# Optimization experiments

Measured on AMD Instinct MI355X. Metric: run time of the kernel, lower is better.

The kernel has to match this reference:

```python
import jax, jax.numpy as jnp
import numpy as np

EPS = 1e-5

def _hdc_branch(emb, w, b, dil, ln_g, ln_b):
    # emb: [N, L, E]; w: [K, E, F] ('WIO'); same-length dilated conv
    y = jax.lax.conv_general_dilated(
        emb, w, window_strides=(1,), padding=[(dil, dil)],
        rhs_dilation=(dil,), dimension_numbers=('NWC', 'WIO', 'NWC')) + b
    m = y.mean(-1, keepdims=True)
    v = ((y - m) ** 2).mean(-1, keepdims=True)
    y = (y - m) / jnp.sqrt(v + EPS) * ln_g + ln_b
    return jax.nn.relu(y)  # [N, L, F]

def _news_encoder(titles, embedding, w1, b1, w2, b2, w3, b3, ln_g, ln_b,
                  q_levels, q_words):
    B, n, L = titles.shape
    E = embedding.shape[-1]
    emb = embedding[titles].reshape(B * n, L, E)  # dropout = identity (eval)
    d = jnp.stack([
        _hdc_branch(emb, w1, b1, 1, ln_g, ln_b),
        _hdc_branch(emb, w2, b2, 2, ln_g, ln_b),
        _hdc_branch(emb, w3, b3, 3, ln_g, ln_b),
    ], axis=2)  # [Bn, L, 3, F]
    F = d.shape[-1]
    d = d.reshape(B, n, L, 3, F)
    scale = jnp.sqrt(jnp.asarray(E, d.dtype))  # original divides by sqrt(embedding_dim)
    # level-wise attention pooling (1-row query over 3 levels)
    wl = jax.nn.softmax(jnp.einsum('f,bnlkf->bnlk', q_levels[0], d) / scale, axis=-1)
    attn = jnp.einsum('bnlk,bnlkf->bnlf', wl, d)  # [B, n, L, F]
    # word-wise attention pooling (1-row query over L words)
    ww = jax.nn.softmax(jnp.einsum('f,bnlf->bnl', q_words[0], attn) / scale, axis=-1)
    reprs = jnp.einsum('bnl,bnlf->bnf', ww, attn)  # [B, n, F]
    return reprs

def setup_inputs() -> dict:
    key = jax.random.key(0)
    ks = jax.random.split(key, 12)
    V, E, F, H = 50000, 300, 150, 50
    return {
        'candidate_title': jax.random.randint(ks[0], (64, 5, 30), 0, V),
        'clicked_title': jax.random.randint(ks[1], (64, H, 30), 0, V),
        'embedding': jax.random.normal(ks[2], (V, E), jnp.float32),
        'w1': jax.random.normal(ks[3], (3, E, F), jnp.float32) * 0.05,
        'b1': jax.random.normal(ks[4], (F,), jnp.float32) * 0.05,
        'w2': jax.random.normal(ks[5], (3, E, F), jnp.float32) * 0.05,
        'b2': jax.random.normal(ks[6], (F,), jnp.float32) * 0.05,
        'w3': jax.random.normal(ks[7], (3, E, F), jnp.float32) * 0.05,
        'b3': jax.random.normal(ks[8], (F,), jnp.float32) * 0.05,
        'ln_g': jnp.ones((F,), jnp.float32),
        'ln_b': jnp.zeros((F,), jnp.float32),
        'q_levels': jax.random.normal(ks[9], (1, F), jnp.float32),
        'q_words': jax.random.normal(ks[10], (1, F), jnp.float32),
        'ltr_w': jax.random.normal(ks[11], (1, H), jnp.float32) * 0.1,
        'ltr_b': jnp.zeros((1,), jnp.float32),
    }

def reference(candidate_title, clicked_title, embedding, w1, b1, w2, b2, w3, b3,
              ln_g, ln_b, q_levels, q_words, ltr_w, ltr_b):
    cdd = _news_encoder(candidate_title, embedding, w1, b1, w2, b2, w3, b3,
                        ln_g, ln_b, q_levels, q_words)  # [B, cdd, F]
    his = _news_encoder(clicked_title, embedding, w1, b1, w2, b2, w3, b3,
                        ln_g, ln_b, q_levels, q_words)  # [B, his, F]
    scores = jnp.einsum('bcf,bhf->bch', cdd, his)        # [B, cdd, his]
    logits = jnp.einsum('bch,oh->bco', scores, ltr_w)[..., 0] + ltr_b[0]  # [B, cdd]
    return jax.nn.log_softmax(logits, axis=1)  # cdd_size > 1 branch
```

## Files before the change

kernel.cpp:

```cpp
#include <hip/hip_runtime.h>

typedef unsigned short u16;
typedef unsigned int   u32;
typedef __bf16 bf16x8 __attribute__((ext_vector_type(8)));
typedef float  f32x4  __attribute__((ext_vector_type(4)));
typedef _Float16 h2 __attribute__((ext_vector_type(2)));

#define M_ROWS 50000
#define M_PAD  50176
#define M_TILES 196
#define N_REAL 1368
#define N_PAD  1536
#define N_TILES 11
#define K_DIM  300
#define K_PAD  320
#define KT     10
#define TROW   1408
#define SEG    152
#define YCOL   152
#define TS     136

#define GLDS(gp, lp) __builtin_amdgcn_global_load_lds( \
    (const __attribute__((address_space(1))) void*)(gp), \
    (__attribute__((address_space(3))) void*)(lp), 16, 0, 0)

static __device__ __forceinline__ u16 f2bf(float x){
  union { float f; u32 u; } a; a.f = x;
  u32 r = a.u + 0x7fffu + ((a.u >> 16) & 1u);
  return (u16)(r >> 16);
}
static __device__ __forceinline__ u16 f2h(float x){
  _Float16 h = (_Float16)x;
  u16 r; __builtin_memcpy(&r, &h, 2); return r;
}
static __device__ __forceinline__ float h2f(u16 v){
  _Float16 h; __builtin_memcpy(&h, &v, 2); return (float)h;
}

static __device__ __forceinline__ float wsum63(float x){
  asm volatile(
    "s_nop 1\n\t"
    "v_add_f32 %0, %0, %0 row_shr:1 bound_ctrl:0\n\t"
    "s_nop 1\n\t"
    "v_add_f32 %0, %0, %0 row_shr:2 bound_ctrl:0\n\t"
    "s_nop 1\n\t"
    "v_add_f32 %0, %0, %0 row_shr:4 bound_ctrl:0\n\t"
    "s_nop 1\n\t"
    "v_add_f32 %0, %0, %0 row_shr:8 bound_ctrl:0\n\t"
    "s_nop 1\n\t"
    "v_add_f32 %0, %0, %0 row_bcast:15 row_mask:0xa\n\t"
    "s_nop 1\n\t"
    "v_add_f32 %0, %0, %0 row_bcast:31 row_mask:0xc\n\t"
    "s_nop 1"
    : "+v"(x));
  return x;
}
static __device__ __forceinline__ float wmax63(float x){
  asm volatile(
    "s_nop 1\n\t"
    "v_max_f32 %0, %0, %0 row_shr:1\n\t"
    "s_nop 1\n\t"
    "v_max_f32 %0, %0, %0 row_shr:2\n\t"
    "s_nop 1\n\t"
    "v_max_f32 %0, %0, %0 row_shr:4\n\t"
    "s_nop 1\n\t"
    "v_max_f32 %0, %0, %0 row_shr:8\n\t"
    "s_nop 1\n\t"
    "v_max_f32 %0, %0, %0 row_bcast:15 row_mask:0xa\n\t"
    "s_nop 1\n\t"
    "v_max_f32 %0, %0, %0 row_bcast:31 row_mask:0xc\n\t"
    "s_nop 1"
    : "+v"(x));
  return x;
}
static __device__ __forceinline__ float rdl63(float x){
  union { float f; int i; } a; a.f = x;
  union { int i; float f; } r; r.i = __builtin_amdgcn_readlane(a.i, 63);
  return r.f;
}

__global__ __launch_bounds__(256) void build_A(const float* __restrict__ emb, u16* __restrict__ A){
  int t = blockIdx.x * 256 + threadIdx.x;
  if (t >= M_PAD * 40) return;
  int m = t / 40, kg = t % 40;
  int k0 = kg * 8;
  int kt = kg >> 2, kgl = kg & 3;
  int tile = m >> 8, ml = m & 255, mb = ml >> 4, row = ml & 15;
  size_t off = ((size_t)tile * KT + kt) * 8192 + mb * 512 + kgl * 128 + row * 8;
  union { uint4 q; u16 s[8]; } p;
  if (m < M_ROWS && k0 + 8 <= K_DIM){
    const float4* src = (const float4*)(emb + (size_t)m * K_DIM + k0);
    float4 v0 = src[0], v1 = src[1];
    p.s[0] = f2bf(v0.x); p.s[1] = f2bf(v0.y); p.s[2] = f2bf(v0.z); p.s[3] = f2bf(v0.w);
    p.s[4] = f2bf(v1.x); p.s[5] = f2bf(v1.y); p.s[6] = f2bf(v1.z); p.s[7] = f2bf(v1.w);
  } else {
    #pragma unroll
    for (int j = 0; j < 8; ++j){
      int k = k0 + j;
      float x = (m < M_ROWS && k < K_DIM) ? emb[(size_t)m * K_DIM + k] : 0.f;
      p.s[j] = f2bf(x);
    }
  }
  *(uint4*)(A + off) = p.q;
}

__global__ void build_B(const float* __restrict__ w1, const float* __restrict__ w2,
                        const float* __restrict__ w3, u16* __restrict__ B){
  int t = blockIdx.x * 256 + threadIdx.x;
  if (t >= N_PAD * K_PAD) return;
  int n = t / K_PAD, k = t % K_PAD;
  float x = 0.f;
  if (n < N_REAL && k < K_DIM){
    int br = n / 456, rem = n % 456, tap = rem / 152, f = rem % 152;
    if (f < 150){
      const float* w = (br == 0) ? w1 : ((br == 1) ? w2 : w3);
      x = w[(tap * K_DIM + k) * 150 + f];
    }
  }
  int tn = n >> 7, nl = n & 127, nb = nl >> 4, col = nl & 15;
  int kt = k >> 5, kl = k & 31, kg = kl >> 3, k8 = kl & 7;
  B[((size_t)tn * KT + kt) * 4096 + nb * 512 + kg * 128 + col * 8 + k8] = f2bf(x);
}

__global__ __launch_bounds__(512, 4) void gemm_k(const u16* __restrict__ A, const u16* __restrict__ B,
                                                 u16* __restrict__ T){
  __shared__ __align__(16) u16 lds[24576];
  u16* lA = lds;
  u16* lB = lds + 16384;
  const int flat = blockIdx.x;
  const int xcd = flat & 7, ord = flat >> 3;
  const int wg = (xcd < 4) ? (xcd * 270 + ord) : (1080 + (xcd - 4) * 269 + ord);
  const int tn = wg % 11, tileM = wg / 11;
  const int tid = threadIdx.x, wave = tid >> 6, lane = tid & 63;
  const int wm = wave >> 1, wn = wave & 1;
  f32x4 acc[4][4];
  #pragma unroll
  for (int i = 0; i < 4; ++i)
    #pragma unroll
    for (int j = 0; j < 4; ++j) acc[i][j] = (f32x4){0.f, 0.f, 0.f, 0.f};
  const u16* Ab = A + (size_t)tileM * KT * 8192;
  const u16* Bb = B + (size_t)tn * KT * 4096;
  for (int rd = 0; rd < 5; ++rd){
    __syncthreads();
    #pragma unroll
    for (int j = 0; j < 4; ++j)
      GLDS(Ab + rd * 16384 + j * 4096 + tid * 8, lA + j * 4096 + tid * 8);
    #pragma unroll
    for (int j = 0; j < 2; ++j)
      GLDS(Bb + rd * 8192 + j * 4096 + tid * 8, lB + j * 4096 + tid * 8);
    __syncthreads();
    #pragma unroll
    for (int kk = 0; kk < 2; ++kk){
      const bf16x8* A8 = (const bf16x8*)(lA + kk * 8192);
      const bf16x8* B8 = (const bf16x8*)(lB + kk * 4096);
      bf16x8 av[4], bv[4];
      #pragma unroll
      for (int i = 0; i < 4; ++i) av[i] = A8[(wm * 4 + i) * 64 + lane];
      #pragma unroll
      for (int j = 0; j < 4; ++j) bv[j] = B8[(wn * 4 + j) * 64 + lane];
      #pragma unroll
      for (int i = 0; i < 4; ++i)
        #pragma unroll
        for (int j = 0; j < 4; ++j)
          acc[i][j] = __builtin_amdgcn_mfma_f32_16x16x32_bf16(av[i], bv[j], acc[i][j], 0, 0, 0);
    }
  }
  const int r0 = (lane >> 4) * 4, c0 = lane & 15;
  const int row = tid >> 2, q = tid & 3;
  #pragma unroll
  for (int half = 0; half < 2; ++half){
    __syncthreads();
    if ((wm >> 1) == half){
      const int rbase = (wm & 1) * 64;
      #pragma unroll
      for (int i = 0; i < 4; ++i){
        #pragma unroll
        for (int j = 0; j < 4; ++j){
          int col = wn * 64 + j * 16 + c0;
          #pragma unroll
          for (int r = 0; r < 4; ++r)
            lds[(rbase + i * 16 + r0 + r) * TS + col] = f2h(acc[i][j][r]);
        }
      }
    }
    __syncthreads();
    int m = tileM * 256 + half * 128 + row;
    if (m < M_ROWS){
      const u16* src = lds + row * TS + q * 32;
      u16* dst = T + (size_t)m * TROW + tn * 128 + q * 32;
      uint4 v0 = *(const uint4*)(src);
      uint4 v1 = *(const uint4*)(src + 8);
      uint4 v2 = *(const uint4*)(src + 16);
      uint4 v3 = *(const uint4*)(src + 24);
      *(uint4*)(dst)      = v0;
      *(uint4*)(dst + 8)  = v1;
      *(uint4*)(dst + 16) = v2;
      *(uint4*)(dst + 24) = v3;
    }
  }
}

__global__ __launch_bounds__(512, 8) void encode_k(
    const int* __restrict__ cand, const int* __restrict__ clk,
    const u16* __restrict__ T,
    const float* __restrict__ b1, const float* __restrict__ b2, const float* __restrict__ b3,
    const float* __restrict__ lng, const float* __restrict__ lnb,
    const float* __restrict__ ql, const float* __restrict__ qw,
    float* __restrict__ rc, float* __restrict__ rh){
  __shared__ __align__(16) u16 ybuf[90][YCOL];
  __shared__ float tl[32];
  __shared__ float pbuf[8][YCOL];
  __shared__ u32 wordoff[30];
  const int t = blockIdx.x;
  const int tid = threadIdx.x, wave = tid >> 6, lane = tid & 63;
  const int* wp; float* outp;
  if (t < 320){ wp = cand + t * 30;                outp = rc + t * 150; }
  else        { wp = clk + (size_t)(t - 320) * 30; outp = rh + (size_t)(t - 320) * 150; }
  if (tid < 30) wordoff[tid] = (u32)wp[tid] * (u32)TROW;
  __syncthreads();
  const float invs = 0.057735026918962576f;
  const int f0 = lane, f1 = lane + 64, f2 = lane + 128;
  const bool has2 = (f2 < 150);

  #pragma unroll
  for (int it = 0; it < 4; ++it){
    int item = tid + it * 512;
    if (item < 1710){
      int p = item / 19, fg = item - p * 19;
      int l = p / 3, br = p - l * 3, dil = br + 1;
      union { uint4 q; h2 h[4]; } s; s.q = (uint4){0u, 0u, 0u, 0u};
      #pragma unroll
      for (int tap = 0; tap < 3; ++tap){
        int ls = l + (tap - 1) * dil;
        if (ls >= 0 && ls < 30){
          union { uint4 q; h2 h[4]; } v;
          v.q = *(const uint4*)(T + wordoff[ls] + br * 456 + tap * SEG + fg * 8);
          #pragma unroll
          for (int i = 0; i < 4; ++i) s.h[i] += v.h[i];
        }
      }
      *(uint4*)&ybuf[p][fg * 8] = s.q;
    }
  }

  float qlv0 = ql[f0], qlv1 = ql[f1], qlv2 = has2 ? ql[f2] : 0.f;
  float qwv0 = qw[f0], qwv1 = qw[f1], qwv2 = has2 ? qw[f2] : 0.f;
  float lg0 = lng[f0], lg1 = lng[f1], lg2 = has2 ? lng[f2] : 0.f;
  float lb0 = lnb[f0], lb1 = lnb[f1], lb2 = has2 ? lnb[f2] : 0.f;
  float bs[3][3];
  {
    const float* bl[3] = {b1, b2, b3};
    #pragma unroll
    for (int br = 0; br < 3; ++br){
      bs[br][0] = bl[br][f0]; bs[br][1] = bl[br][f1]; bs[br][2] = has2 ? bl[br][f2] : 0.f;
    }
  }
  __syncthreads();

  float at0[4], at1[4], at2[4]; int myl[4]; int nw = 0;
  for (int l = wave; l < 30; l += 8){
    float dr[3][3]; float lvl[3];
    #pragma unroll
    for (int br = 0; br < 3; ++br){
      int p = l * 3 + br;
      float y0 = h2f(ybuf[p][f0]) + bs[br][0];
      float y1 = h2f(ybuf[p][f1]) + bs[br][1];
      float y2 = has2 ? (h2f(ybuf[p][f2]) + bs[br][2]) : 0.f;
      float s  = y0 + y1 + y2;
      float ss = y0 * y0 + y1 * y1 + y2 * y2;
      float st = wsum63(s), sst = wsum63(ss);
      float mean = rdl63(st) * (1.f / 150.f);
      float var  = rdl63(sst) * (1.f / 150.f) - mean * mean;
      float rstd = rsqrtf(var + 1e-5f);
      float d0 = fmaxf((y0 - mean) * rstd * lg0 + lb0, 0.f);
      float d1 = fmaxf((y1 - mean) * rstd * lg1 + lb1, 0.f);
      float d2 = has2 ? fmaxf((y2 - mean) * rstd * lg2 + lb2, 0.f) : 0.f;
      dr[br][0] = d0; dr[br][1] = d1; dr[br][2] = d2;
      float dot = qlv0 * d0 + qlv1 * d1 + qlv2 * d2;
      lvl[br] = rdl63(wsum63(dot)) * invs;
    }
    float mx = fmaxf(lvl[0], fmaxf(lvl[1], lvl[2]));
    float e0 = __expf(lvl[0] - mx), e1 = __expf(lvl[1] - mx), e2 = __expf(lvl[2] - mx);
    float inv = 1.f / (e0 + e1 + e2);
    float w0 = e0 * inv, w1v = e1 * inv, w2v = e2 * inv;
    float a0 = w0 * dr[0][0] + w1v * dr[1][0] + w2v * dr[2][0];
    float a1 = w0 * dr[0][1] + w1v * dr[1][1] + w2v * dr[2][1];
    float a2 = w0 * dr[0][2] + w1v * dr[1][2] + w2v * dr[2][2];
    float dot = qwv0 * a0 + qwv1 * a1 + qwv2 * a2;
    float tw = wsum63(dot);
    if (lane == 63) tl[l] = tw * invs;
    at0[nw] = a0; at1[nw] = a1; at2[nw] = a2; myl[nw] = l; ++nw;
  }
  __syncthreads();

  if (wave == 0){
    float v = (lane < 30) ? tl[lane] : -1e30f;
    float mx = rdl63(wmax63(v));
    float e = (lane < 30) ? __expf(v - mx) : 0.f;
    float den = rdl63(wsum63(e));
    if (lane < 30) tl[lane] = e / den;
  }
  __syncthreads();

  float p0 = 0.f, p1 = 0.f, p2 = 0.f;
  for (int q = 0; q < nw; ++q){
    float wwv = tl[myl[q]];
    p0 += wwv * at0[q]; p1 += wwv * at1[q]; p2 += wwv * at2[q];
  }
  pbuf[wave][lane] = p0;
  pbuf[wave][lane + 64] = p1;
  if (has2) pbuf[wave][lane + 128] = p2;
  __syncthreads();
  if (tid < 150){
    float acc = 0.f;
    #pragma unroll
    for (int w = 0; w < 8; ++w) acc += pbuf[w][tid];
    outp[tid] = acc;
  }
}

__global__ __launch_bounds__(256) void final_k(const float* __restrict__ rc, const float* __restrict__ rh,
                                               const float* __restrict__ lw, const float* __restrict__ lb,
                                               float* __restrict__ out){
  __shared__ float Cl[750];
  __shared__ float Hl[7500];
  __shared__ float sc[5][52];
  __shared__ float lg[5];
  const int b = blockIdx.x, tid = threadIdx.x;
  const float* C = rc + b * 750;
  const float* H = rh + (size_t)b * 7500;
  for (int i = tid; i < 750; i += 256) Cl[i] = C[i];
  for (int i = tid; i < 7500; i += 256) Hl[i] = H[i];
  __syncthreads();
  if (tid < 250){
    int c = tid / 50, h = tid % 50;
    float s = 0.f;
    #pragma unroll 10
    for (int k = 0; k < 150; ++k) s += Cl[c * 150 + k] * Hl[h * 150 + k];
    sc[c][h] = s;
  }
  __syncthreads();
  if (tid < 5){
    float s = lb[0];
    for (int h = 0; h < 50; ++h) s += sc[tid][h] * lw[h];
    lg[tid] = s;
  }
  __syncthreads();
  if (tid < 5){
    float mx = fmaxf(fmaxf(fmaxf(lg[0], lg[1]), fmaxf(lg[2], lg[3])), lg[4]);
    float den = 0.f;
    for (int c = 0; c < 5; ++c) den += expf(lg[c] - mx);
    out[b * 5 + tid] = lg[tid] - mx - logf(den);
  }
}

extern "C" void kernel_launch(void* const* d_in, const int* in_sizes, int n_in,
                              void* d_out, int out_size, void* d_ws, size_t ws_size,
                              hipStream_t stream){
  const int*   cand = (const int*)d_in[0];
  const int*   clk  = (const int*)d_in[1];
  const float* emb  = (const float*)d_in[2];
  const float* w1   = (const float*)d_in[3];
  const float* b1   = (const float*)d_in[4];
  const float* w2   = (const float*)d_in[5];
  const float* b2   = (const float*)d_in[6];
  const float* w3   = (const float*)d_in[7];
  const float* b3   = (const float*)d_in[8];
  const float* lng  = (const float*)d_in[9];
  const float* lnb  = (const float*)d_in[10];
  const float* ql   = (const float*)d_in[11];
  const float* qw   = (const float*)d_in[12];
  const float* lw   = (const float*)d_in[13];
  const float* lb   = (const float*)d_in[14];
  float* out = (float*)d_out;

  char* ws = (char*)d_ws;
  const size_t szA = (size_t)M_TILES * KT * 16384;
  const size_t szB = (size_t)12 * KT * 8192;
  const size_t szT = (size_t)M_ROWS * TROW * 2;
  u16*   A  = (u16*)ws;
  u16*   B  = (u16*)(ws + szA);
  u16*   T  = (u16*)(ws + szA + szB);
  float* rc = (float*)(ws + szA + szB + szT);
  float* rh = rc + 320 * 150;

  build_A<<<(M_PAD * 40 + 255) / 256, 256, 0, stream>>>(emb, A);
  build_B<<<(N_PAD * K_PAD + 255) / 256, 256, 0, stream>>>(w1, w2, w3, B);
  gemm_k<<<dim3(N_TILES * M_TILES), 512, 0, stream>>>(A, B, T);
  encode_k<<<3520, 512, 0, stream>>>(cand, clk, T, b1, b2, b3, lng, lnb, ql, qw, rc, rh);
  final_k<<<64, 256, 0, stream>>>(rc, rh, lw, lb, out);
}
```

Measured before the change: 296.9 us.

## Double-buffer LDS in GEMM to overlap global loads with MFMA

Replaces the 5-round load-then-compute loop in the embedding×weight GEMM with a 10-stage ping-pong LDS pipeline. The next K-slice is issued with global_load_lds while the current one is consumed, and a manual vmcnt wait plus barrier gates each stage. This is meant to hide global memory latency behind the MFMA work. The cost is more barriers per tile and smaller per-stage loads, and the hand-written waitcnt has to match the load count exactly.

New measurement: 297.3 us. No clear change (+0.1%).

```diff
diff --git a/kernel.cpp b/kernel.cpp
--- a/kernel.cpp
+++ b/kernel.cpp
@@ -125,8 +125,6 @@
 __global__ __launch_bounds__(512, 4) void gemm_k(const u16* __restrict__ A, const u16* __restrict__ B,
                                                  u16* __restrict__ T){
   __shared__ __align__(16) u16 lds[24576];
-  u16* lA = lds;
-  u16* lB = lds + 16384;
   const int flat = blockIdx.x;
   const int xcd = flat & 7, ord = flat >> 3;
   const int wg = (xcd < 4) ? (xcd * 270 + ord) : (1080 + (xcd - 4) * 269 + ord);
@@ -140,30 +138,36 @@
     for (int j = 0; j < 4; ++j) acc[i][j] = (f32x4){0.f, 0.f, 0.f, 0.f};
   const u16* Ab = A + (size_t)tileM * KT * 8192;
   const u16* Bb = B + (size_t)tn * KT * 4096;
-  for (int rd = 0; rd < 5; ++rd){
-    __syncthreads();
-    #pragma unroll
-    for (int j = 0; j < 4; ++j)
-      GLDS(Ab + rd * 16384 + j * 4096 + tid * 8, lA + j * 4096 + tid * 8);
-    #pragma unroll
-    for (int j = 0; j < 2; ++j)
-      GLDS(Bb + rd * 8192 + j * 4096 + tid * 8, lB + j * 4096 + tid * 8);
-    __syncthreads();
-    #pragma unroll
-    for (int kk = 0; kk < 2; ++kk){
-      const bf16x8* A8 = (const bf16x8*)(lA + kk * 8192);
-      const bf16x8* B8 = (const bf16x8*)(lB + kk * 4096);
-      bf16x8 av[4], bv[4];
+  GLDS(Ab + tid * 8,        lds + tid * 8);
+  GLDS(Ab + 4096 + tid * 8, lds + 4096 + tid * 8);
+  GLDS(Bb + tid * 8,        lds + 8192 + tid * 8);
+  #pragma unroll
+  for (int s = 0; s < 10; ++s){
+    const int b = s & 1;
+    if (s < 9){
+      u16* dst = lds + (b ^ 1) * 12288;
+      GLDS(Ab + (s + 1) * 8192 + tid * 8,        dst + tid * 8);
+      GLDS(Ab + (s + 1) * 8192 + 4096 + tid * 8, dst + 4096 + tid * 8);
+      GLDS(Bb + (s + 1) * 4096 + tid * 8,        dst + 8192 + tid * 8);
+      asm volatile("s_waitcnt vmcnt(3)" ::: "memory");
+    } else {
+      asm volatile("s_waitcnt vmcnt(0)" ::: "memory");
+    }
+    __builtin_amdgcn_sched_barrier(0);
+    __builtin_amdgcn_s_barrier();
+    const bf16x8* A8 = (const bf16x8*)(lds + b * 12288);
+    const bf16x8* B8 = (const bf16x8*)(lds + b * 12288 + 8192);
+    bf16x8 av[4], bv[4];
+    #pragma unroll
+    for (int i = 0; i < 4; ++i) av[i] = A8[(wm * 4 + i) * 64 + lane];
+    #pragma unroll
+    for (int j = 0; j < 4; ++j) bv[j] = B8[(wn * 4 + j) * 64 + lane];
+    #pragma unroll
+    for (int i = 0; i < 4; ++i)
       #pragma unroll
-      for (int i = 0; i < 4; ++i) av[i] = A8[(wm * 4 + i) * 64 + lane];
-      #pragma unroll
-      for (int j = 0; j < 4; ++j) bv[j] = B8[(wn * 4 + j) * 64 + lane];
-      #pragma unroll
-      for (int i = 0; i < 4; ++i)
-        #pragma unroll
-        for (int j = 0; j < 4; ++j)
-          acc[i][j] = __builtin_amdgcn_mfma_f32_16x16x32_bf16(av[i], bv[j], acc[i][j], 0, 0, 0);
-    }
+      for (int j = 0; j < 4; ++j)
+        acc[i][j] = __builtin_amdgcn_mfma_f32_16x16x32_bf16(av[i], bv[j], acc[i][j], 0, 0, 0);
+    __builtin_amdgcn_s_barrier();
   }
   const int r0 = (lane >> 4) * 4, c0 = lane & 15;
   const int row = tid >> 2, q = tid & 3;
```
